# Optimization experiments

Hardware: AMD Instinct MI355X
Metric: run time of the kernel (lower is better)

The kernel has to match this reference:

```python
import jax, jax.numpy as jnp
import numpy as np

B, M, S, F, E, H, L = 4, 10, 1024, 128, 512, 8, 6
DH = E // H
NV, NP = 6, 3
LN_EPS = 1e-5


def _ln(x, g, b):
    mu = x.mean(-1, keepdims=True)
    var = ((x - mu) ** 2).mean(-1, keepdims=True)
    return (x - mu) * jax.lax.rsqrt(var + LN_EPS) * g + b


def setup_inputs() -> dict:
    key = jax.random.key(0)
    ks = jax.random.split(key, 24)
    sc = 0.02
    inp = {
        'features': jax.random.normal(ks[0], (B, M, S, F), jnp.float32),
        'target': jax.random.normal(ks[1], (B, S, NV), jnp.float32),
        'step_idx': jax.random.randint(ks[2], (B,), 0, 40),
        'day_of_year': jax.random.randint(ks[3], (B,), 0, 365),
        'emb_W': jax.random.normal(ks[4], (F, E), jnp.float32) * sc,
        'emb_b': jnp.zeros((E,), jnp.float32),
        'station_emb': jax.random.uniform(ks[5], (S + 1, E), jnp.float32),
        'Wq': jax.random.normal(ks[6], (L, E, E), jnp.float32) * sc,
        'Wk': jax.random.normal(ks[7], (L, E, E), jnp.float32) * sc,
        'Wv': jax.random.normal(ks[8], (L, E, E), jnp.float32) * sc,
        'attn_W': jax.random.normal(ks[9], (L, E, E), jnp.float32) * sc,
        'attn_b': jnp.zeros((L, E), jnp.float32),
        'ln_attn_g': jnp.ones((L, E), jnp.float32),
        'ln_attn_b': jnp.zeros((L, E), jnp.float32),
        'ffn_W1': jax.random.normal(ks[10], (L, E, E), jnp.float32) * sc,
        'ffn_b1': jnp.zeros((L, E), jnp.float32),
        'ffn_W2': jax.random.normal(ks[11], (L, E, E), jnp.float32) * sc,
        'ffn_b2': jnp.zeros((L, E), jnp.float32),
        'ln1_g': jnp.ones((L, E), jnp.float32),
        'ln1_b': jnp.zeros((L, E), jnp.float32),
        'ln2_g': jnp.ones((L, E), jnp.float32),
        'ln2_b': jnp.zeros((L, E), jnp.float32),
        'reg_W': jax.random.normal(ks[12], (E, NV * NP), jnp.float32) * sc,
        'reg_b': jnp.zeros((NV * NP,), jnp.float32),
    }
    return inp


def reference(features, target, step_idx, day_of_year, emb_W, emb_b, station_emb,
              Wq, Wk, Wv, attn_W, attn_b, ln_attn_g, ln_attn_b,
              ffn_W1, ffn_b1, ffn_W2, ffn_b2, ln1_g, ln1_b, ln2_g, ln2_b,
              reg_W, reg_b):
    # embedding + mean over ensemble members (select_member='mean')
    emb = features @ emb_W + emb_b            # [B,M,S,E]
    x = emb.mean(axis=1)                      # [B,S,E]

    # station embedding lookup; stations with any NaN target get index -1 (last row)
    sid = jnp.broadcast_to(jnp.arange(S), (B, S))
    has_no_obs = jnp.isnan(target).any(axis=-1)
    sid = jnp.where(has_no_obs, -1, sid)
    x = x + station_emb[sid]                  # [B,S,E]

    scale = jnp.sqrt(jnp.float32(DH))
    for i in range(L):
        # multi-head attention; NOTE: original softmax is over dim=0 (batch)
        q = (x @ Wq[i]).reshape(B, S, H, DH)
        k = (x @ Wk[i]).reshape(B, S, H, DH)
        v = (x @ Wv[i]).reshape(B, S, H, DH)
        att = jnp.einsum('bqhd,bkhd->hbqk', q, k) / scale   # [H,B,S,S]
        att = jax.nn.softmax(att, axis=1)                   # softmax over batch dim, per original
        o = jnp.einsum('hbqk,bkhd->bqhd', att, v).reshape(B, S, E)
        o = o @ attn_W[i] + attn_b[i]
        o = jax.nn.silu(_ln(o, ln_attn_g[i], ln_attn_b[i]))
        # block: LN -> FFN -> residual -> LN (dropout = 0)
        h = _ln(o, ln1_g[i], ln1_b[i])
        f = jax.nn.silu(h @ ffn_W1[i] + ffn_b1[i]) @ ffn_W2[i] + ffn_b2[i]
        x = _ln(f + h, ln2_g[i], ln2_b[i])

    out = x @ reg_W + reg_b                   # [B,S,NV*NP]
    return out.reshape(B, S, NV, NP)
```

## Files before the change

kernel.cpp:

```cpp
#include <hip/hip_runtime.h>
#include <stdint.h>

typedef float   f32x4 __attribute__((ext_vector_type(4)));
typedef float   f32x2 __attribute__((ext_vector_type(2)));
typedef __bf16  bfx8  __attribute__((ext_vector_type(8)));
typedef uint16_t u16x8 __attribute__((ext_vector_type(8)));

#define AS1(p) ((__attribute__((address_space(1))) void*)(p))
#define AS3(p) ((__attribute__((address_space(3))) void*)(p))

__device__ __forceinline__ uint16_t f2bf(float f) {
    union { float f; uint32_t u; } c; c.f = f;
    uint32_t u = c.u;
    return (uint16_t)((u + 0x7FFFu + ((u >> 16) & 1u)) >> 16);
}
__device__ __forceinline__ float bf2f(uint16_t v) {
    union { uint32_t u; float f; } c; c.u = ((uint32_t)v) << 16; return c.f;
}
__device__ __forceinline__ float sigmoidf_(float x) { return 1.0f / (1.0f + __expf(-x)); }
__device__ __forceinline__ float frcp(float x) { float r; asm("v_rcp_f32 %0, %1" : "=v"(r) : "v"(x)); return r; }
__device__ __forceinline__ void bar_lds() {
    asm volatile("s_waitcnt lgkmcnt(0)" ::: "memory");
    __builtin_amdgcn_s_barrier();
}

__global__ __launch_bounds__(256) void wconv_k(
    const float* __restrict__ Wq, const float* __restrict__ Wk, const float* __restrict__ Wv,
    const float* __restrict__ Wo, const float* __restrict__ W1, const float* __restrict__ W2,
    const float* __restrict__ Wemb, uint16_t* __restrict__ arena)
{
    __shared__ uint16_t tl[64][65];
    const int z = blockIdx.z;
    const float* in; uint16_t* out; int K, N;
    if (z < 36) {
        const int type = z / 6, l = z % 6;
        const float* bases[6] = {Wq, Wk, Wv, Wo, W1, W2};
        in = bases[type] + (size_t)l * 512 * 512;
        K = 512; N = 512;
        if (type < 3) out = arena + (size_t)l * 786432u + (size_t)type * 262144u;
        else          out = arena + 4718592u + (size_t)(type - 3) * 1572864u + (size_t)l * 262144u;
    } else {
        if (blockIdx.y >= 2) return;
        in = Wemb; K = 128; N = 512;
        out = arena + 9437184u;
    }
    const int n0 = blockIdx.x * 64, k0 = blockIdx.y * 64;
    const int t = threadIdx.x, r = t >> 2, seg = t & 3;
    const float* src = in + (size_t)(k0 + r) * N + n0 + seg * 16;
#pragma unroll
    for (int v2 = 0; v2 < 4; ++v2) {
        f32x4 d = *(const f32x4*)(src + v2 * 4);
#pragma unroll
        for (int j = 0; j < 4; ++j) tl[r][seg * 16 + v2 * 4 + j] = f2bf(d[j]);
    }
    __syncthreads();
    u16x8 o0, o1;
#pragma unroll
    for (int j = 0; j < 8; ++j) { o0[j] = tl[seg * 16 + j][r]; o1[j] = tl[seg * 16 + 8 + j][r]; }
    uint16_t* dst = out + (size_t)(n0 + r) * K + k0 + seg * 16;
    *(u16x8*)dst = o0; *(u16x8*)(dst + 8) = o1;
}

__global__ __launch_bounds__(256) void fmean_k(const float* __restrict__ feat, uint16_t* __restrict__ fm)
{
    int id = blockIdx.x * 256 + threadIdx.x;
    int f = id & 127, row = id >> 7;
    int b = row >> 10, s = row & 1023;
    float acc = 0.f;
#pragma unroll
    for (int m = 0; m < 10; ++m)
        acc += feat[(size_t)((b * 10 + m) * 1024 + s) * 128 + f];
    fm[id] = f2bf(acc * 0.1f);
}

__global__ __launch_bounds__(256) void station_k(const float* __restrict__ target,
    const float* __restrict__ semb, const float* __restrict__ emb32, uint16_t* __restrict__ x16)
{
    int row = blockIdx.x;
    int s = row & 1023;
    bool bad = false;
#pragma unroll
    for (int v = 0; v < 6; ++v) bad = bad || isnan(target[(size_t)row * 6 + v]);
    int sid = bad ? 1024 : s;
    const float* se = semb + (size_t)sid * 512;
    for (int c = threadIdx.x; c < 512; c += 256) {
        float val = emb32[(size_t)row * 512 + c] + se[c];
        x16[(size_t)row * 512 + c] = f2bf(val);
    }
}

template<int BIAS, int SILU, int OUTBF, int KMOD>
__global__ __launch_bounds__(256) void gemm64(const uint16_t* __restrict__ A,
    const uint16_t* __restrict__ Bw, const float* __restrict__ bias,
    void* __restrict__ Cout, int Msz, int Nsz, int Ksz)
{
    __shared__ uint16_t lA[64 * 64];
    __shared__ uint16_t lB[64 * 64];
    const int t = threadIdx.x;
    const int lane = t & 63, w = t >> 6;
    const int wm = (w >> 1) * 32, wn = (w & 1) * 32;
    const int m0 = blockIdx.y * 64, n0 = blockIdx.x * 64;
    const int l15 = lane & 15, l4 = lane >> 4;
    char* lAb = (char*)lA; char* lBb = (char*)lB;
    const int srow = lane >> 3, sseg = lane & 7;
    f32x4 acc[2][2] = {};
    for (int k0 = 0; k0 < Ksz; k0 += 64) {
        const size_t bstride = KMOD ? 512 : (size_t)Ksz;
        const int bk0 = KMOD ? (k0 & 511) : k0;
#pragma unroll
        for (int i = 0; i < 2; ++i) {
            int row = w * 16 + i * 8 + srow;
            const char* ga = (const char*)A + ((size_t)(m0 + row) * Ksz + k0) * 2 + sseg * 16;
            __builtin_amdgcn_global_load_lds(AS1(ga), AS3(lAb + (w * 16 + i * 8) * 128), 16, 0, 0);
            const char* gb = (const char*)Bw + ((size_t)(n0 + row) * bstride + bk0) * 2 + sseg * 16;
            __builtin_amdgcn_global_load_lds(AS1(gb), AS3(lBb + (w * 16 + i * 8) * 128), 16, 0, 0);
        }
        __syncthreads();
#pragma unroll
        for (int kf = 0; kf < 2; ++kf) {
            bfx8 af[2], bf2[2];
#pragma unroll
            for (int mf = 0; mf < 2; ++mf)
                af[mf] = *(const bfx8*)(lAb + (wm + mf * 16 + l15) * 128 + kf * 64 + l4 * 16);
#pragma unroll
            for (int nf = 0; nf < 2; ++nf)
                bf2[nf] = *(const bfx8*)(lBb + (wn + nf * 16 + l15) * 128 + kf * 64 + l4 * 16);
#pragma unroll
            for (int mf = 0; mf < 2; ++mf)
#pragma unroll
                for (int nf = 0; nf < 2; ++nf)
                    acc[mf][nf] = __builtin_amdgcn_mfma_f32_16x16x32_bf16(af[mf], bf2[nf], acc[mf][nf], 0, 0, 0);
        }
        __syncthreads();
    }
#pragma unroll
    for (int mf = 0; mf < 2; ++mf)
#pragma unroll
        for (int nf = 0; nf < 2; ++nf)
#pragma unroll
            for (int r = 0; r < 4; ++r) {
                int row = m0 + wm + mf * 16 + l4 * 4 + r;
                int col = n0 + wn + nf * 16 + l15;
                float v = acc[mf][nf][r];
                if (BIAS) v += bias[col];
                if (SILU) v = v * sigmoidf_(v);
                if (OUTBF) ((uint16_t*)Cout)[(size_t)row * Nsz + col] = f2bf(v);
                else       ((float*)Cout)[(size_t)row * Nsz + col] = v;
            }
}

__global__ __launch_bounds__(256) void gemm128(const uint16_t* __restrict__ A,
    const uint16_t* __restrict__ Bw, uint16_t* __restrict__ Cout, int Nsz, int Ksz)
{
    __shared__ uint16_t lA[128 * 64];
    __shared__ uint16_t lB[128 * 64];
    const int t = threadIdx.x;
    const int lane = t & 63, w = t >> 6;
    const int wm = (w >> 1) * 64, wn = (w & 1) * 64;
    const int m0 = blockIdx.y * 128, n0 = blockIdx.x * 128;
    const int l15 = lane & 15, l4 = lane >> 4;
    char* lAb = (char*)lA; char* lBb = (char*)lB;
    const int srow = lane >> 3, sseg = lane & 7;
    f32x4 acc[4][4] = {};
    for (int k0 = 0; k0 < Ksz; k0 += 64) {
#pragma unroll
        for (int i = 0; i < 4; ++i) {
            int row = w * 32 + i * 8 + srow;
            const char* ga = (const char*)A + ((size_t)(m0 + row) * Ksz + k0) * 2 + sseg * 16;
            __builtin_amdgcn_global_load_lds(AS1(ga), AS3(lAb + (w * 32 + i * 8) * 128), 16, 0, 0);
            const char* gb = (const char*)Bw + ((size_t)(n0 + row) * Ksz + k0) * 2 + sseg * 16;
            __builtin_amdgcn_global_load_lds(AS1(gb), AS3(lBb + (w * 32 + i * 8) * 128), 16, 0, 0);
        }
        __syncthreads();
#pragma unroll
        for (int kf = 0; kf < 2; ++kf) {
            bfx8 af[4], bf2[4];
#pragma unroll
            for (int mf = 0; mf < 4; ++mf)
                af[mf] = *(const bfx8*)(lAb + (wm + mf * 16 + l15) * 128 + kf * 64 + l4 * 16);
#pragma unroll
            for (int nf = 0; nf < 4; ++nf)
                bf2[nf] = *(const bfx8*)(lBb + (wn + nf * 16 + l15) * 128 + kf * 64 + l4 * 16);
#pragma unroll
            for (int mf = 0; mf < 4; ++mf)
#pragma unroll
                for (int nf = 0; nf < 4; ++nf)
                    acc[mf][nf] = __builtin_amdgcn_mfma_f32_16x16x32_bf16(af[mf], bf2[nf], acc[mf][nf], 0, 0, 0);
        }
        __syncthreads();
    }
#pragma unroll
    for (int mf = 0; mf < 4; ++mf)
#pragma unroll
        for (int nf = 0; nf < 4; ++nf)
#pragma unroll
            for (int r = 0; r < 4; ++r) {
                int row = m0 + wm + mf * 16 + l4 * 4 + r;
                int col = n0 + wn + nf * 16 + l15;
                Cout[(size_t)row * Nsz + col] = f2bf(acc[mf][nf][r]);
            }
}

__global__ __launch_bounds__(256) void vtrans_k(const uint16_t* __restrict__ qkv, uint16_t* __restrict__ vt)
{
    __shared__ uint16_t tl[64][65];
    const int bh = blockIdx.y;
    const int s0 = blockIdx.x * 64;
    const int b = bh >> 3, h = bh & 7;
    const int t = threadIdx.x, r = t >> 2, seg = t & 3;
    const uint16_t* src = qkv + (size_t)(b * 1024 + s0 + r) * 1536 + 1024 + h * 64 + seg * 16;
    u16x8 a0 = *(const u16x8*)src;
    u16x8 a1 = *(const u16x8*)(src + 8);
#pragma unroll
    for (int j = 0; j < 8; ++j) { tl[r][seg * 16 + j] = a0[j]; tl[r][seg * 16 + 8 + j] = a1[j]; }
    __syncthreads();
    u16x8 o0, o1;
#pragma unroll
    for (int j = 0; j < 8; ++j) { o0[j] = tl[seg * 16 + j][r]; o1[j] = tl[seg * 16 + 8 + j][r]; }
    uint16_t* dst = vt + (size_t)(bh * 64 + r) * 1024 + s0 + seg * 16;
    *(u16x8*)dst = o0; *(u16x8*)(dst + 8) = o1;
}

__global__ __launch_bounds__(512, 4) void attn_k(const uint16_t* __restrict__ qkv,
    const uint16_t* __restrict__ vt, uint16_t* __restrict__ o16)
{
    __shared__ __align__(16) char smem[33792 + 16384];
    float*    sS  = (float*)smem;
    uint16_t* sPb = (uint16_t*)(smem + 33792);
    float*    sO  = (float*)smem;

    const int t = threadIdx.x;
    const int lane = t & 63, w = t >> 6;
    const int b = w & 3, kg = w >> 2;
    const int bid = blockIdx.x;
    const int h = bid & 7, qt = (bid >> 3) & 31, ks = bid >> 8;
    const int q0 = qt * 32;
    const int l15 = lane & 15, l4 = lane >> 4;

    bfx8 qa[2][2];
#pragma unroll
    for (int mf = 0; mf < 2; ++mf)
#pragma unroll
        for (int kf = 0; kf < 2; ++kf)
            qa[mf][kf] = *(const bfx8*)(qkv + (size_t)(b * 1024 + q0 + mf * 16 + l15) * 1536 + h * 64 + kf * 32 + l4 * 8);

    const int kbase = ks * 512 + kg * 256;
    f32x4 oacc[2][4] = {};
    for (int it = 0; it < 8; ++it) {
        const int k0 = kbase + it * 32;
        bfx8 kb[2][2], vb[4];
#pragma unroll
        for (int nf = 0; nf < 4; ++nf)
            vb[nf] = *(const bfx8*)(vt + (size_t)((b * 8 + h) * 64 + nf * 16 + l15) * 1024 + k0 + l4 * 8);
#pragma unroll
        for (int nf = 0; nf < 2; ++nf)
#pragma unroll
            for (int kf = 0; kf < 2; ++kf)
                kb[nf][kf] = *(const bfx8*)(qkv + (size_t)(b * 1024 + k0 + nf * 16 + l15) * 1536 + 512 + h * 64 + kf * 32 + l4 * 8);
        f32x4 sacc[2][2] = {};
#pragma unroll
        for (int kf = 0; kf < 2; ++kf)
#pragma unroll
            for (int mf = 0; mf < 2; ++mf)
#pragma unroll
                for (int nf = 0; nf < 2; ++nf)
                    sacc[mf][nf] = __builtin_amdgcn_mfma_f32_16x16x32_bf16(qa[mf][kf], kb[nf][kf], sacc[mf][nf], 0, 0, 0);
#pragma unroll
        for (int mf = 0; mf < 2; ++mf)
#pragma unroll
            for (int nf = 0; nf < 2; ++nf)
#pragma unroll
                for (int r = 0; r < 4; ++r)
                    sS[((b * 2 + kg) * 32 + mf * 16 + l4 * 4 + r) * 33 + nf * 16 + l15] = sacc[mf][nf][r] * 0.125f;
        bar_lds();
#pragma unroll
        for (int jj = 0; jj < 4; ++jj) {
            int e = jj * 512 + t;
            int kg2 = e >> 10, q = (e >> 5) & 31, k = e & 31;
            int base = (kg2 * 32 + q) * 33 + k;
            float s0v = sS[base], s1v = sS[base + 2112], s2v = sS[base + 4224], s3v = sS[base + 6336];
            float mx = fmaxf(fmaxf(s0v, s1v), fmaxf(s2v, s3v));
            float e0 = __expf(s0v - mx), e1 = __expf(s1v - mx);
            float e2 = __expf(s2v - mx), e3 = __expf(s3v - mx);
            float inv = frcp(e0 + e1 + e2 + e3);
            int sw = (q * 64 + k * 2) ^ ((q & 3) << 4);
            char* pb = (char*)sPb + kg2 * 2048 + sw;
            *(uint16_t*)(pb)         = f2bf(e0 * inv);
            *(uint16_t*)(pb + 4096)  = f2bf(e1 * inv);
            *(uint16_t*)(pb + 8192)  = f2bf(e2 * inv);
            *(uint16_t*)(pb + 12288) = f2bf(e3 * inv);
        }
        bar_lds();
        bfx8 pa[2];
#pragma unroll
        for (int mf = 0; mf < 2; ++mf) {
            int row = mf * 16 + l15;
            pa[mf] = *(const bfx8*)((char*)sPb + (b * 2 + kg) * 2048 + ((row * 64 + l4 * 16) ^ ((row & 3) << 4)));
        }
#pragma unroll
        for (int mf = 0; mf < 2; ++mf)
#pragma unroll
            for (int nf = 0; nf < 4; ++nf)
                oacc[mf][nf] = __builtin_amdgcn_mfma_f32_16x16x32_bf16(pa[mf], vb[nf], oacc[mf][nf], 0, 0, 0);
    }
    bar_lds();
    if (kg == 1) {
#pragma unroll
        for (int mf = 0; mf < 2; ++mf)
#pragma unroll
            for (int nf = 0; nf < 4; ++nf)
#pragma unroll
                for (int r = 0; r < 4; ++r)
                    sO[(b * 32 + mf * 16 + l4 * 4 + r) * 64 + nf * 16 + l15] = oacc[mf][nf][r];
    }
    bar_lds();
    if (kg == 0) {
#pragma unroll
        for (int mf = 0; mf < 2; ++mf)
#pragma unroll
            for (int nf = 0; nf < 4; ++nf)
#pragma unroll
                for (int r = 0; r < 4; ++r) {
                    float v = oacc[mf][nf][r] + sO[(b * 32 + mf * 16 + l4 * 4 + r) * 64 + nf * 16 + l15];
                    o16[(size_t)(b * 1024 + q0 + mf * 16 + l4 * 4 + r) * 1024 + ks * 512 + h * 64 + nf * 16 + l15] = f2bf(v);
                }
    }
}

__global__ __launch_bounds__(64) void ln_fuse_k(const float* __restrict__ in,
    const float* __restrict__ g1, const float* __restrict__ b1,
    const float* __restrict__ g2, const float* __restrict__ b2,
    float* __restrict__ h32, uint16_t* __restrict__ h16)
{
    const int row = blockIdx.x, lane = threadIdx.x;
    const float* p = in + (size_t)row * 512 + lane * 8;
    f32x4 a = *(const f32x4*)p, bvec = *(const f32x4*)(p + 4);
    float x[8] = {a[0], a[1], a[2], a[3], bvec[0], bvec[1], bvec[2], bvec[3]};
    float sum = 0.f, sq = 0.f;
#pragma unroll
    for (int i = 0; i < 8; ++i) { sum += x[i]; sq += x[i] * x[i]; }
    for (int m = 32; m; m >>= 1) { sum += __shfl_xor(sum, m); sq += __shfl_xor(sq, m); }
    float mu = sum * (1.f / 512.f);
    float rs = rsqrtf(sq * (1.f / 512.f) - mu * mu + 1e-5f);
    float y[8]; float s2 = 0.f, q2 = 0.f;
#pragma unroll
    for (int i = 0; i < 8; ++i) {
        int c = lane * 8 + i;
        float v = (x[i] - mu) * rs * g1[c] + b1[c];
        v = v * sigmoidf_(v);
        y[i] = v; s2 += v; q2 += v * v;
    }
    for (int m = 32; m; m >>= 1) { s2 += __shfl_xor(s2, m); q2 += __shfl_xor(q2, m); }
    float mu2 = s2 * (1.f / 512.f);
    float rs2 = rsqrtf(q2 * (1.f / 512.f) - mu2 * mu2 + 1e-5f);
#pragma unroll
    for (int i = 0; i < 8; ++i) {
        int c = lane * 8 + i;
        float v = (y[i] - mu2) * rs2 * g2[c] + b2[c];
        h32[(size_t)row * 512 + c] = v;
        h16[(size_t)row * 512 + c] = f2bf(v);
    }
}

__global__ __launch_bounds__(64) void ln_res_k(const float* __restrict__ f, const float* __restrict__ hres,
    const float* __restrict__ g, const float* __restrict__ bb, uint16_t* __restrict__ x16)
{
    const int row = blockIdx.x, lane = threadIdx.x;
    const size_t base = (size_t)row * 512 + lane * 8;
    f32x4 a = *(const f32x4*)(f + base), b2v = *(const f32x4*)(f + base + 4);
    f32x4 ha = *(const f32x4*)(hres + base), hb = *(const f32x4*)(hres + base + 4);
    float x[8] = {a[0] + ha[0], a[1] + ha[1], a[2] + ha[2], a[3] + ha[3],
                  b2v[0] + hb[0], b2v[1] + hb[1], b2v[2] + hb[2], b2v[3] + hb[3]};
    float sum = 0.f, sq = 0.f;
#pragma unroll
    for (int i = 0; i < 8; ++i) { sum += x[i]; sq += x[i] * x[i]; }
    for (int m = 32; m; m >>= 1) { sum += __shfl_xor(sum, m); sq += __shfl_xor(sq, m); }
    float mu = sum * (1.f / 512.f);
    float rs = rsqrtf(sq * (1.f / 512.f) - mu * mu + 1e-5f);
#pragma unroll
    for (int i = 0; i < 8; ++i) {
        int c = lane * 8 + i;
        float v = (x[i] - mu) * rs * g[c] + bb[c];
        x16[base + i] = f2bf(v);
    }
}

__global__ __launch_bounds__(256) void reg_k(const uint16_t* __restrict__ x16, const float* __restrict__ W,
    const float* __restrict__ bb, float* __restrict__ out)
{
    const int gid = blockIdx.x * 256 + threadIdx.x;
    const int row = gid >> 3, kq = gid & 7;
    const uint16_t* xp = x16 + (size_t)row * 512 + kq * 64;
    float acc[18];
#pragma unroll
    for (int j = 0; j < 18; ++j) acc[j] = 0.f;
    for (int k0 = 0; k0 < 64; k0 += 8) {
        u16x8 xv = *(const u16x8*)(xp + k0);
#pragma unroll
        for (int kk = 0; kk < 8; ++kk) {
            const float* wr = W + (size_t)(kq * 64 + k0 + kk) * 18;
            f32x4 w0 = *(const f32x4*)(wr);
            f32x4 w1 = *(const f32x4*)(wr + 4);
            f32x4 w2 = *(const f32x4*)(wr + 8);
            f32x4 w3 = *(const f32x4*)(wr + 12);
            f32x2 w4 = *(const f32x2*)(wr + 16);
            float xs = bf2f(xv[kk]);
#pragma unroll
            for (int j = 0; j < 4; ++j) acc[j] += xs * w0[j];
#pragma unroll
            for (int j = 0; j < 4; ++j) acc[4 + j] += xs * w1[j];
#pragma unroll
            for (int j = 0; j < 4; ++j) acc[8 + j] += xs * w2[j];
#pragma unroll
            for (int j = 0; j < 4; ++j) acc[12 + j] += xs * w3[j];
            acc[16] += xs * w4[0];
            acc[17] += xs * w4[1];
        }
    }
#pragma unroll
    for (int j = 0; j < 18; ++j) {
        acc[j] += __shfl_xor(acc[j], 1);
        acc[j] += __shfl_xor(acc[j], 2);
        acc[j] += __shfl_xor(acc[j], 4);
    }
    if (kq == 0) {
#pragma unroll
        for (int j = 0; j < 18; ++j)
            out[(size_t)row * 18 + j] = acc[j] + bb[j];
    }
}

extern "C" void kernel_launch(void* const* d_in, const int* in_sizes, int n_in,
                              void* d_out, int out_size, void* d_ws, size_t ws_size,
                              hipStream_t stream)
{
    const float* features = (const float*)d_in[0];
    const float* target   = (const float*)d_in[1];
    const float* emb_W    = (const float*)d_in[4];
    const float* emb_b    = (const float*)d_in[5];
    const float* station  = (const float*)d_in[6];
    const float* Wq   = (const float*)d_in[7];
    const float* Wk   = (const float*)d_in[8];
    const float* Wv   = (const float*)d_in[9];
    const float* Wo   = (const float*)d_in[10];
    const float* attn_b = (const float*)d_in[11];
    const float* lng  = (const float*)d_in[12];
    const float* lnb  = (const float*)d_in[13];
    const float* W1   = (const float*)d_in[14];
    const float* b1   = (const float*)d_in[15];
    const float* W2   = (const float*)d_in[16];
    const float* b2   = (const float*)d_in[17];
    const float* ln1g = (const float*)d_in[18];
    const float* ln1b = (const float*)d_in[19];
    const float* ln2g = (const float*)d_in[20];
    const float* ln2b = (const float*)d_in[21];
    const float* regW = (const float*)d_in[22];
    const float* regb = (const float*)d_in[23];
    float* out = (float*)d_out;

    const size_t NEEDED = 73531392;
    if (ws_size < NEEDED) return;

    char* ws = (char*)d_ws;
    uint16_t* wt   = (uint16_t*)(ws);
    uint16_t* x16  = (uint16_t*)(ws + 19005440);
    uint16_t* qkv  = (uint16_t*)(ws + 23199744);
    uint16_t* vt   = (uint16_t*)(ws + 35782656);
    uint16_t* o16  = (uint16_t*)(ws + 39976960);
    float*    t32  = (float*)(ws + 48365568);
    float*    h32  = (float*)(ws + 56754176);
    uint16_t* h16  = (uint16_t*)(ws + 65142784);
    uint16_t* f16  = (uint16_t*)(ws + 69337088);
    uint16_t* fm16 = (uint16_t*)(ws + 56754176);

    wconv_k<<<dim3(8, 8, 37), 256, 0, stream>>>(Wq, Wk, Wv, Wo, W1, W2, emb_W, wt);
    fmean_k<<<dim3(2048), 256, 0, stream>>>(features, fm16);
    gemm64<1, 0, 0, 0><<<dim3(8, 64), 256, 0, stream>>>(fm16, wt + 9437184u, emb_b, t32, 4096, 512, 128);
    station_k<<<dim3(4096), 256, 0, stream>>>(target, station, t32, x16);

    for (int l = 0; l < 6; ++l) {
        gemm128<<<dim3(12, 32), 256, 0, stream>>>(x16, wt + (size_t)l * 786432u, qkv, 1536, 512);
        vtrans_k<<<dim3(16, 32), 256, 0, stream>>>(qkv, vt);
        attn_k<<<dim3(512), 512, 0, stream>>>(qkv, vt, o16);
        gemm64<1, 0, 0, 1><<<dim3(8, 64), 256, 0, stream>>>(o16, wt + 4718592u + (size_t)l * 262144u, attn_b + l * 512, t32, 4096, 512, 1024);
        ln_fuse_k<<<dim3(4096), 64, 0, stream>>>(t32, lng + l * 512, lnb + l * 512, ln1g + l * 512, ln1b + l * 512, h32, h16);
        gemm64<1, 1, 1, 0><<<dim3(8, 64), 256, 0, stream>>>(h16, wt + 6291456u + (size_t)l * 262144u, b1 + l * 512, f16, 4096, 512, 512);
        gemm64<1, 0, 0, 0><<<dim3(8, 64), 256, 0, stream>>>(f16, wt + 7864320u + (size_t)l * 262144u, b2 + l * 512, t32, 4096, 512, 512);
        ln_res_k<<<dim3(4096), 64, 0, stream>>>(t32, h32, ln2g + l * 512, ln2b + l * 512, x16);
    }
    reg_k<<<dim3(128), 256, 0, stream>>>(x16, regW, regb, out);
}
```

Measured before the change: 687.3 us.

## Register-resident batch-softmax attention, double-buffered GEMMs, fuse regression into final LN

Attention is rewritten so one 64-lane wave computes scores for all four batches of a 16-query tile. The batch-dim softmax is done in registers, and probabilities feed MFMA as the B operand via packed bf16 conversion. This removes the LDS staging and barriers of the previous attention. Both GEMM kernels double-buffer their LDS tiles to prefetch the next K slice while computing. The regression head is fused into the last LN+residual kernel, which removes a launch and a round trip of x16. The trade-off is higher LDS use, more registers per wave in attention, and possible ordering risks in the prefetch.

```diff
diff --git a/kernel.cpp b/kernel.cpp
--- a/kernel.cpp
+++ b/kernel.cpp
@@ -5,6 +5,7 @@
 typedef float   f32x2 __attribute__((ext_vector_type(2)));
 typedef __bf16  bfx8  __attribute__((ext_vector_type(8)));
 typedef uint16_t u16x8 __attribute__((ext_vector_type(8)));
+typedef uint16_t u16x4 __attribute__((ext_vector_type(4)));
 
 #define AS1(p) ((__attribute__((address_space(1))) void*)(p))
 #define AS3(p) ((__attribute__((address_space(3))) void*)(p))
@@ -14,14 +15,10 @@
     uint32_t u = c.u;
     return (uint16_t)((u + 0x7FFFu + ((u >> 16) & 1u)) >> 16);
 }
-__device__ __forceinline__ float bf2f(uint16_t v) {
-    union { uint32_t u; float f; } c; c.u = ((uint32_t)v) << 16; return c.f;
-}
 __device__ __forceinline__ float sigmoidf_(float x) { return 1.0f / (1.0f + __expf(-x)); }
 __device__ __forceinline__ float frcp(float x) { float r; asm("v_rcp_f32 %0, %1" : "=v"(r) : "v"(x)); return r; }
-__device__ __forceinline__ void bar_lds() {
-    asm volatile("s_waitcnt lgkmcnt(0)" ::: "memory");
-    __builtin_amdgcn_s_barrier();
+__device__ __forceinline__ uint32_t cvtpk(float lo, float hi) {
+    uint32_t r; asm("v_cvt_pk_bf16_f32 %0, %1, %2" : "=v"(r) : "v"(lo), "v"(hi)); return r;
 }
 
 __global__ __launch_bounds__(256) void wconv_k(
@@ -94,37 +91,46 @@
     const uint16_t* __restrict__ Bw, const float* __restrict__ bias,
     void* __restrict__ Cout, int Msz, int Nsz, int Ksz)
 {
-    __shared__ uint16_t lA[64 * 64];
-    __shared__ uint16_t lB[64 * 64];
+    __shared__ uint16_t lA[2][64 * 64];
+    __shared__ uint16_t lB[2][64 * 64];
     const int t = threadIdx.x;
     const int lane = t & 63, w = t >> 6;
     const int wm = (w >> 1) * 32, wn = (w & 1) * 32;
     const int m0 = blockIdx.y * 64, n0 = blockIdx.x * 64;
     const int l15 = lane & 15, l4 = lane >> 4;
-    char* lAb = (char*)lA; char* lBb = (char*)lB;
     const int srow = lane >> 3, sseg = lane & 7;
-    f32x4 acc[2][2] = {};
-    for (int k0 = 0; k0 < Ksz; k0 += 64) {
+
+    auto stage = [&](int buf, int k0) {
         const size_t bstride = KMOD ? 512 : (size_t)Ksz;
         const int bk0 = KMOD ? (k0 & 511) : k0;
+        char* lab = (char*)lA[buf]; char* lbb = (char*)lB[buf];
 #pragma unroll
         for (int i = 0; i < 2; ++i) {
             int row = w * 16 + i * 8 + srow;
             const char* ga = (const char*)A + ((size_t)(m0 + row) * Ksz + k0) * 2 + sseg * 16;
-            __builtin_amdgcn_global_load_lds(AS1(ga), AS3(lAb + (w * 16 + i * 8) * 128), 16, 0, 0);
+            __builtin_amdgcn_global_load_lds(AS1(ga), AS3(lab + (w * 16 + i * 8) * 128), 16, 0, 0);
             const char* gb = (const char*)Bw + ((size_t)(n0 + row) * bstride + bk0) * 2 + sseg * 16;
-            __builtin_amdgcn_global_load_lds(AS1(gb), AS3(lBb + (w * 16 + i * 8) * 128), 16, 0, 0);
-        }
-        __syncthreads();
+            __builtin_amdgcn_global_load_lds(AS1(gb), AS3(lbb + (w * 16 + i * 8) * 128), 16, 0, 0);
+        }
+    };
+
+    f32x4 acc[2][2] = {};
+    const int nk = Ksz >> 6;
+    stage(0, 0);
+    __syncthreads();
+    for (int i = 0; i < nk; ++i) {
+        if (i + 1 < nk) stage((i + 1) & 1, (i + 1) * 64);
+        const char* lab = (const char*)lA[i & 1];
+        const char* lbb = (const char*)lB[i & 1];
 #pragma unroll
         for (int kf = 0; kf < 2; ++kf) {
             bfx8 af[2], bf2[2];
 #pragma unroll
             for (int mf = 0; mf < 2; ++mf)
-                af[mf] = *(const bfx8*)(lAb + (wm + mf * 16 + l15) * 128 + kf * 64 + l4 * 16);
+                af[mf] = *(const bfx8*)(lab + (wm + mf * 16 + l15) * 128 + kf * 64 + l4 * 16);
 #pragma unroll
             for (int nf = 0; nf < 2; ++nf)
-                bf2[nf] = *(const bfx8*)(lBb + (wn + nf * 16 + l15) * 128 + kf * 64 + l4 * 16);
+                bf2[nf] = *(const bfx8*)(lbb + (wn + nf * 16 + l15) * 128 + kf * 64 + l4 * 16);
 #pragma unroll
             for (int mf = 0; mf < 2; ++mf)
 #pragma unroll
@@ -152,35 +158,44 @@
 __global__ __launch_bounds__(256) void gemm128(const uint16_t* __restrict__ A,
     const uint16_t* __restrict__ Bw, uint16_t* __restrict__ Cout, int Nsz, int Ksz)
 {
-    __shared__ uint16_t lA[128 * 64];
-    __shared__ uint16_t lB[128 * 64];
+    __shared__ uint16_t lA[2][128 * 64];
+    __shared__ uint16_t lB[2][128 * 64];
     const int t = threadIdx.x;
     const int lane = t & 63, w = t >> 6;
     const int wm = (w >> 1) * 64, wn = (w & 1) * 64;
     const int m0 = blockIdx.y * 128, n0 = blockIdx.x * 128;
     const int l15 = lane & 15, l4 = lane >> 4;
-    char* lAb = (char*)lA; char* lBb = (char*)lB;
     const int srow = lane >> 3, sseg = lane & 7;
-    f32x4 acc[4][4] = {};
-    for (int k0 = 0; k0 < Ksz; k0 += 64) {
+
+    auto stage = [&](int buf, int k0) {
+        char* lab = (char*)lA[buf]; char* lbb = (char*)lB[buf];
 #pragma unroll
         for (int i = 0; i < 4; ++i) {
             int row = w * 32 + i * 8 + srow;
             const char* ga = (const char*)A + ((size_t)(m0 + row) * Ksz + k0) * 2 + sseg * 16;
-            __builtin_amdgcn_global_load_lds(AS1(ga), AS3(lAb + (w * 32 + i * 8) * 128), 16, 0, 0);
+            __builtin_amdgcn_global_load_lds(AS1(ga), AS3(lab + (w * 32 + i * 8) * 128), 16, 0, 0);
             const char* gb = (const char*)Bw + ((size_t)(n0 + row) * Ksz + k0) * 2 + sseg * 16;
-            __builtin_amdgcn_global_load_lds(AS1(gb), AS3(lBb + (w * 32 + i * 8) * 128), 16, 0, 0);
-        }
-        __syncthreads();
+            __builtin_amdgcn_global_load_lds(AS1(gb), AS3(lbb + (w * 32 + i * 8) * 128), 16, 0, 0);
+        }
+    };
+
+    f32x4 acc[4][4] = {};
+    const int nk = Ksz >> 6;
+    stage(0, 0);
+    __syncthreads();
+    for (int i = 0; i < nk; ++i) {
+        if (i + 1 < nk) stage((i + 1) & 1, (i + 1) * 64);
+        const char* lab = (const char*)lA[i & 1];
+        const char* lbb = (const char*)lB[i & 1];
 #pragma unroll
         for (int kf = 0; kf < 2; ++kf) {
             bfx8 af[4], bf2[4];
 #pragma unroll
             for (int mf = 0; mf < 4; ++mf)
-                af[mf] = *(const bfx8*)(lAb + (wm + mf * 16 + l15) * 128 + kf * 64 + l4 * 16);
+                af[mf] = *(const bfx8*)(lab + (wm + mf * 16 + l15) * 128 + kf * 64 + l4 * 16);
 #pragma unroll
             for (int nf = 0; nf < 4; ++nf)
-                bf2[nf] = *(const bfx8*)(lBb + (wn + nf * 16 + l15) * 128 + kf * 64 + l4 * 16);
+                bf2[nf] = *(const bfx8*)(lbb + (wn + nf * 16 + l15) * 128 + kf * 64 + l4 * 16);
 #pragma unroll
             for (int mf = 0; mf < 4; ++mf)
 #pragma unroll
@@ -221,110 +236,83 @@
     *(u16x8*)dst = o0; *(u16x8*)(dst + 8) = o1;
 }
 
-__global__ __launch_bounds__(512, 4) void attn_k(const uint16_t* __restrict__ qkv,
+__global__ __launch_bounds__(64) void attn_k(const uint16_t* __restrict__ qkv,
     const uint16_t* __restrict__ vt, uint16_t* __restrict__ o16)
 {
-    __shared__ __align__(16) char smem[33792 + 16384];
-    float*    sS  = (float*)smem;
-    uint16_t* sPb = (uint16_t*)(smem + 33792);
-    float*    sO  = (float*)smem;
-
-    const int t = threadIdx.x;
-    const int lane = t & 63, w = t >> 6;
-    const int b = w & 3, kg = w >> 2;
+    const int lane = threadIdx.x;
+    const int l15 = lane & 15, l4 = lane >> 4;
     const int bid = blockIdx.x;
-    const int h = bid & 7, qt = (bid >> 3) & 31, ks = bid >> 8;
-    const int q0 = qt * 32;
-    const int l15 = lane & 15, l4 = lane >> 4;
-
-    bfx8 qa[2][2];
-#pragma unroll
-    for (int mf = 0; mf < 2; ++mf)
+    const int h = bid & 7, qt = (bid >> 3) & 63, ks = bid >> 9;
+    const int q0 = qt * 16;
+
+    bfx8 qa[4][2];
+#pragma unroll
+    for (int b = 0; b < 4; ++b)
 #pragma unroll
         for (int kf = 0; kf < 2; ++kf)
-            qa[mf][kf] = *(const bfx8*)(qkv + (size_t)(b * 1024 + q0 + mf * 16 + l15) * 1536 + h * 64 + kf * 32 + l4 * 8);
-
-    const int kbase = ks * 512 + kg * 256;
-    f32x4 oacc[2][4] = {};
-    for (int it = 0; it < 8; ++it) {
+            qa[b][kf] = *(const bfx8*)(qkv + (size_t)(b * 1024 + q0 + l15) * 1536 + h * 64 + kf * 32 + l4 * 8);
+
+    f32x4 oacc[4][4] = {};
+    const int kbase = ks * 512;
+    for (int it = 0; it < 16; ++it) {
         const int k0 = kbase + it * 32;
-        bfx8 kb[2][2], vb[4];
-#pragma unroll
-        for (int nf = 0; nf < 4; ++nf)
-            vb[nf] = *(const bfx8*)(vt + (size_t)((b * 8 + h) * 64 + nf * 16 + l15) * 1024 + k0 + l4 * 8);
-#pragma unroll
-        for (int nf = 0; nf < 2; ++nf)
-#pragma unroll
-            for (int kf = 0; kf < 2; ++kf)
-                kb[nf][kf] = *(const bfx8*)(qkv + (size_t)(b * 1024 + k0 + nf * 16 + l15) * 1536 + 512 + h * 64 + kf * 32 + l4 * 8);
-        f32x4 sacc[2][2] = {};
-#pragma unroll
-        for (int kf = 0; kf < 2; ++kf)
-#pragma unroll
-            for (int mf = 0; mf < 2; ++mf)
-#pragma unroll
-                for (int nf = 0; nf < 2; ++nf)
-                    sacc[mf][nf] = __builtin_amdgcn_mfma_f32_16x16x32_bf16(qa[mf][kf], kb[nf][kf], sacc[mf][nf], 0, 0, 0);
-#pragma unroll
-        for (int mf = 0; mf < 2; ++mf)
-#pragma unroll
-            for (int nf = 0; nf < 2; ++nf)
-#pragma unroll
-                for (int r = 0; r < 4; ++r)
-                    sS[((b * 2 + kg) * 32 + mf * 16 + l4 * 4 + r) * 33 + nf * 16 + l15] = sacc[mf][nf][r] * 0.125f;
-        bar_lds();
-#pragma unroll
-        for (int jj = 0; jj < 4; ++jj) {
-            int e = jj * 512 + t;
-            int kg2 = e >> 10, q = (e >> 5) & 31, k = e & 31;
-            int base = (kg2 * 32 + q) * 33 + k;
-            float s0v = sS[base], s1v = sS[base + 2112], s2v = sS[base + 4224], s3v = sS[base + 6336];
-            float mx = fmaxf(fmaxf(s0v, s1v), fmaxf(s2v, s3v));
-            float e0 = __expf(s0v - mx), e1 = __expf(s1v - mx);
-            float e2 = __expf(s2v - mx), e3 = __expf(s3v - mx);
-            float inv = frcp(e0 + e1 + e2 + e3);
-            int sw = (q * 64 + k * 2) ^ ((q & 3) << 4);
-            char* pb = (char*)sPb + kg2 * 2048 + sw;
-            *(uint16_t*)(pb)         = f2bf(e0 * inv);
-            *(uint16_t*)(pb + 4096)  = f2bf(e1 * inv);
-            *(uint16_t*)(pb + 8192)  = f2bf(e2 * inv);
-            *(uint16_t*)(pb + 12288) = f2bf(e3 * inv);
-        }
-        bar_lds();
-        bfx8 pa[2];
-#pragma unroll
-        for (int mf = 0; mf < 2; ++mf) {
-            int row = mf * 16 + l15;
-            pa[mf] = *(const bfx8*)((char*)sPb + (b * 2 + kg) * 2048 + ((row * 64 + l4 * 16) ^ ((row & 3) << 4)));
-        }
-#pragma unroll
-        for (int mf = 0; mf < 2; ++mf)
-#pragma unroll
-            for (int nf = 0; nf < 4; ++nf)
-                oacc[mf][nf] = __builtin_amdgcn_mfma_f32_16x16x32_bf16(pa[mf], vb[nf], oacc[mf][nf], 0, 0, 0);
-    }
-    bar_lds();
-    if (kg == 1) {
-#pragma unroll
-        for (int mf = 0; mf < 2; ++mf)
-#pragma unroll
-            for (int nf = 0; nf < 4; ++nf)
-#pragma unroll
-                for (int r = 0; r < 4; ++r)
-                    sO[(b * 32 + mf * 16 + l4 * 4 + r) * 64 + nf * 16 + l15] = oacc[mf][nf][r];
-    }
-    bar_lds();
-    if (kg == 0) {
-#pragma unroll
-        for (int mf = 0; mf < 2; ++mf)
-#pragma unroll
-            for (int nf = 0; nf < 4; ++nf)
-#pragma unroll
-                for (int r = 0; r < 4; ++r) {
-                    float v = oacc[mf][nf][r] + sO[(b * 32 + mf * 16 + l4 * 4 + r) * 64 + nf * 16 + l15];
-                    o16[(size_t)(b * 1024 + q0 + mf * 16 + l4 * 4 + r) * 1024 + ks * 512 + h * 64 + nf * 16 + l15] = f2bf(v);
-                }
-    }
+        f32x4 sacc[4][2] = {};
+#pragma unroll
+        for (int b = 0; b < 4; ++b) {
+            bfx8 kb[2][2];
+#pragma unroll
+            for (int kt = 0; kt < 2; ++kt)
+#pragma unroll
+                for (int kf = 0; kf < 2; ++kf)
+                    kb[kt][kf] = *(const bfx8*)(qkv + (size_t)(b * 1024 + k0 + kt * 16 + l15) * 1536 + 512 + h * 64 + kf * 32 + l4 * 8);
+#pragma unroll
+            for (int kt = 0; kt < 2; ++kt)
+#pragma unroll
+                for (int kf = 0; kf < 2; ++kf)
+                    sacc[b][kt] = __builtin_amdgcn_mfma_f32_16x16x32_bf16(kb[kt][kf], qa[b][kf], sacc[b][kt], 0, 0, 0);
+        }
+        float p[2][4][4];
+#pragma unroll
+        for (int kt = 0; kt < 2; ++kt)
+#pragma unroll
+            for (int r = 0; r < 4; ++r) {
+                float s0 = sacc[0][kt][r], s1 = sacc[1][kt][r];
+                float s2 = sacc[2][kt][r], s3 = sacc[3][kt][r];
+                float mx = fmaxf(fmaxf(s0, s1), fmaxf(s2, s3));
+                float e0 = __expf((s0 - mx) * 0.125f);
+                float e1 = __expf((s1 - mx) * 0.125f);
+                float e2 = __expf((s2 - mx) * 0.125f);
+                float e3 = __expf((s3 - mx) * 0.125f);
+                float inv = frcp(e0 + e1 + e2 + e3);
+                p[kt][0][r] = e0 * inv; p[kt][1][r] = e1 * inv;
+                p[kt][2][r] = e2 * inv; p[kt][3][r] = e3 * inv;
+            }
+#pragma unroll
+        for (int b = 0; b < 4; ++b) {
+            union { uint32_t u[4]; bfx8 v; } pf;
+            pf.u[0] = cvtpk(p[0][b][0], p[0][b][1]);
+            pf.u[1] = cvtpk(p[0][b][2], p[0][b][3]);
+            pf.u[2] = cvtpk(p[1][b][0], p[1][b][1]);
+            pf.u[3] = cvtpk(p[1][b][2], p[1][b][3]);
+#pragma unroll
+            for (int m = 0; m < 4; ++m) {
+                const uint16_t* vp = vt + (size_t)((b * 8 + h) * 64 + m * 16 + l15) * 1024 + k0 + 4 * l4;
+                union { u16x4 h2[2]; bfx8 v; } vf;
+                vf.h2[0] = *(const u16x4*)vp;
+                vf.h2[1] = *(const u16x4*)(vp + 16);
+                oacc[b][m] = __builtin_amdgcn_mfma_f32_16x16x32_bf16(vf.v, pf.v, oacc[b][m], 0, 0, 0);
+            }
+        }
+    }
+#pragma unroll
+    for (int b = 0; b < 4; ++b)
+#pragma unroll
+        for (int m = 0; m < 4; ++m) {
+            u16x4 ov;
+#pragma unroll
+            for (int r = 0; r < 4; ++r) ov[r] = f2bf(oacc[b][m][r]);
+            *(u16x4*)(o16 + (size_t)(b * 1024 + q0 + l15) * 1024 + ks * 512 + h * 64 + m * 16 + 4 * l4) = ov;
+        }
 }
 
 __global__ __launch_bounds__(64) void ln_fuse_k(const float* __restrict__ in,
@@ -362,8 +350,10 @@
     }
 }
 
+template<int LAST>
 __global__ __launch_bounds__(64) void ln_res_k(const float* __restrict__ f, const float* __restrict__ hres,
-    const float* __restrict__ g, const float* __restrict__ bb, uint16_t* __restrict__ x16)
+    const float* __restrict__ g, const float* __restrict__ bb, uint16_t* __restrict__ x16,
+    const float* __restrict__ regW, const float* __restrict__ regb, float* __restrict__ out)
 {
     const int row = blockIdx.x, lane = threadIdx.x;
     const size_t base = (size_t)row * 512 + lane * 8;
@@ -377,56 +367,39 @@
     for (int m = 32; m; m >>= 1) { sum += __shfl_xor(sum, m); sq += __shfl_xor(sq, m); }
     float mu = sum * (1.f / 512.f);
     float rs = rsqrtf(sq * (1.f / 512.f) - mu * mu + 1e-5f);
+    float v[8];
 #pragma unroll
     for (int i = 0; i < 8; ++i) {
         int c = lane * 8 + i;
-        float v = (x[i] - mu) * rs * g[c] + bb[c];
-        x16[base + i] = f2bf(v);
-    }
-}
-
-__global__ __launch_bounds__(256) void reg_k(const uint16_t* __restrict__ x16, const float* __restrict__ W,
-    const float* __restrict__ bb, float* __restrict__ out)
-{
-    const int gid = blockIdx.x * 256 + threadIdx.x;
-    const int row = gid >> 3, kq = gid & 7;
-    const uint16_t* xp = x16 + (size_t)row * 512 + kq * 64;
-    float acc[18];
-#pragma unroll
-    for (int j = 0; j < 18; ++j) acc[j] = 0.f;
-    for (int k0 = 0; k0 < 64; k0 += 8) {
-        u16x8 xv = *(const u16x8*)(xp + k0);
-#pragma unroll
-        for (int kk = 0; kk < 8; ++kk) {
-            const float* wr = W + (size_t)(kq * 64 + k0 + kk) * 18;
-            f32x4 w0 = *(const f32x4*)(wr);
-            f32x4 w1 = *(const f32x4*)(wr + 4);
-            f32x4 w2 = *(const f32x4*)(wr + 8);
-            f32x4 w3 = *(const f32x4*)(wr + 12);
-            f32x2 w4 = *(const f32x2*)(wr + 16);
-            float xs = bf2f(xv[kk]);
-#pragma unroll
-            for (int j = 0; j < 4; ++j) acc[j] += xs * w0[j];
-#pragma unroll
-            for (int j = 0; j < 4; ++j) acc[4 + j] += xs * w1[j];
-#pragma unroll
-            for (int j = 0; j < 4; ++j) acc[8 + j] += xs * w2[j];
-#pragma unroll
-            for (int j = 0; j < 4; ++j) acc[12 + j] += xs * w3[j];
-            acc[16] += xs * w4[0];
-            acc[17] += xs * w4[1];
-        }
-    }
-#pragma unroll
-    for (int j = 0; j < 18; ++j) {
-        acc[j] += __shfl_xor(acc[j], 1);
-        acc[j] += __shfl_xor(acc[j], 2);
-        acc[j] += __shfl_xor(acc[j], 4);
-    }
-    if (kq == 0) {
-#pragma unroll
-        for (int j = 0; j < 18; ++j)
-            out[(size_t)row * 18 + j] = acc[j] + bb[j];
+        v[i] = (x[i] - mu) * rs * g[c] + bb[c];
+    }
+    if (!LAST) {
+#pragma unroll
+        for (int i = 0; i < 8; ++i) x16[base + i] = f2bf(v[i]);
+    } else {
+        float acc[18];
+#pragma unroll
+        for (int j = 0; j < 18; ++j) acc[j] = 0.f;
+#pragma unroll
+        for (int i = 0; i < 8; ++i) {
+            const float* wr = regW + (size_t)(lane * 8 + i) * 18;
+#pragma unroll
+            for (int j = 0; j < 18; ++j) acc[j] += v[i] * wr[j];
+        }
+#pragma unroll
+        for (int j = 0; j < 18; ++j) {
+            acc[j] += __shfl_xor(acc[j], 1);
+            acc[j] += __shfl_xor(acc[j], 2);
+            acc[j] += __shfl_xor(acc[j], 4);
+            acc[j] += __shfl_xor(acc[j], 8);
+            acc[j] += __shfl_xor(acc[j], 16);
+            acc[j] += __shfl_xor(acc[j], 32);
+        }
+        if (lane == 0) {
+#pragma unroll
+            for (int j = 0; j < 18; ++j)
+                out[(size_t)row * 18 + j] = acc[j] + regb[j];
+        }
     }
 }
 
@@ -481,12 +454,14 @@
     for (int l = 0; l < 6; ++l) {
         gemm128<<<dim3(12, 32), 256, 0, stream>>>(x16, wt + (size_t)l * 786432u, qkv, 1536, 512);
         vtrans_k<<<dim3(16, 32), 256, 0, stream>>>(qkv, vt);
-        attn_k<<<dim3(512), 512, 0, stream>>>(qkv, vt, o16);
+        attn_k<<<dim3(1024), 64, 0, stream>>>(qkv, vt, o16);
         gemm64<1, 0, 0, 1><<<dim3(8, 64), 256, 0, stream>>>(o16, wt + 4718592u + (size_t)l * 262144u, attn_b + l * 512, t32, 4096, 512, 1024);
         ln_fuse_k<<<dim3(4096), 64, 0, stream>>>(t32, lng + l * 512, lnb + l * 512, ln1g + l * 512, ln1b + l * 512, h32, h16);
         gemm64<1, 1, 1, 0><<<dim3(8, 64), 256, 0, stream>>>(h16, wt + 6291456u + (size_t)l * 262144u, b1 + l * 512, f16, 4096, 512, 512);
         gemm64<1, 0, 0, 0><<<dim3(8, 64), 256, 0, stream>>>(f16, wt + 7864320u + (size_t)l * 262144u, b2 + l * 512, t32, 4096, 512, 512);
-        ln_res_k<<<dim3(4096), 64, 0, stream>>>(t32, h32, ln2g + l * 512, ln2b + l * 512, x16);
-    }
-    reg_k<<<dim3(128), 256, 0, stream>>>(x16, regW, regb, out);
-}
+        if (l < 5)
+            ln_res_k<0><<<dim3(4096), 64, 0, stream>>>(t32, h32, ln2g + l * 512, ln2b + l * 512, x16, regW, regb, out);
+        else
+            ln_res_k<1><<<dim3(4096), 64, 0, stream>>>(t32, h32, ln2g + l * 512, ln2b + l * 512, x16, regW, regb, out);
+    }
+}
```

New measurement: 1.080 ms. 57.2% more time.
